# Optimization experiments

Hardware: AMD Instinct MI355X
Metric: run time of the kernel (lower is better)

The kernel has to match this reference:

```python
import jax, jax.numpy as jnp
import numpy as np

B, M, D = 8192, 64, 256
NEG = -1e9  # masking value for invalid (padded) memory slots


def setup_inputs() -> dict:
    key = jax.random.key(0)
    ks = jax.random.split(key, 8)
    s = 1.0 / np.sqrt(D)  # nn.Linear default init scale
    return {
        "h_tilde": jax.random.normal(ks[0], (B, D), jnp.float32),
        "mem": jax.random.normal(ks[1], (B, M, D), jnp.float32),
        "lengths": jax.random.randint(ks[2], (B,), 0, M + 1, jnp.int32),
        "Wg_w": jax.random.uniform(ks[3], (D, D), jnp.float32, -s, s),
        "Wg_b": jax.random.uniform(ks[4], (D,), jnp.float32, -s, s),
        "Ug_w": jax.random.uniform(ks[5], (D, D), jnp.float32, -s, s),
        "Ug_b": jax.random.uniform(ks[6], (D,), jnp.float32, -s, s),
        "b_g": jnp.zeros((D,), jnp.float32),
    }


def reference(h_tilde, mem, lengths, Wg_w, Wg_b, Ug_w, Ug_b, b_g):
    # valid-slot mask: [B, M]
    valid = jnp.arange(M)[None, :] < lengths[:, None]
    # per-sample attention over ragged memory
    scores = jnp.einsum("bmd,bd->bm", mem, h_tilde)          # [B, M]
    attn = jax.nn.softmax(jnp.where(valid, scores, NEG), axis=1)
    r = jnp.einsum("bm,bmd->bd", attn, mem)                   # [B, D]
    # gated fusion (two Linears + extra bias)
    g = jax.nn.sigmoid(h_tilde @ Wg_w.T + Wg_b + r @ Ug_w.T + Ug_b + b_g)
    fused = g * r + (1.0 - g) * h_tilde
    # empty-memory samples pass through h_tilde unchanged
    has_mem = (lengths > 0)[:, None]
    return jnp.where(has_mem, fused, h_tilde)
```

## Files before the change

### kernel.cpp

```cpp
#include <hip/hip_runtime.h>
#include <hip/hip_bf16.h>

#define BB 8192
#define MM 64
#define DD 256
#define NEGV -1e9f

__global__ __launch_bounds__(256) void attn_kernel(
    const float* __restrict__ h, const float* __restrict__ mem,
    const int* __restrict__ len, float* __restrict__ r_out)
{
    __shared__ __hip_bfloat16 tile[MM * DD];
    __shared__ float score_s[MM];
    __shared__ float attn_s[MM];

    const int b    = blockIdx.x;
    const int t    = threadIdx.x;
    const int lane = t & 63;
    const int wave = t >> 6;
    const int L    = len[b];

    const float4 hv = *reinterpret_cast<const float4*>(h + (size_t)b * DD + 4 * lane);
    const float* mbase = mem + (size_t)b * MM * DD;

    #pragma unroll
    for (int i = 0; i < 16; ++i) {
        const int m = wave * 16 + i;
        const float4 v = *reinterpret_cast<const float4*>(mbase + m * DD + 4 * lane);

        __hip_bfloat162* t2 =
            reinterpret_cast<__hip_bfloat162*>(tile + m * DD + 4 * lane);
        __hip_bfloat162 p0, p1;
        p0.x = __float2bfloat16(v.x); p0.y = __float2bfloat16(v.y);
        p1.x = __float2bfloat16(v.z); p1.y = __float2bfloat16(v.w);
        t2[0] = p0; t2[1] = p1;

        float p = v.x * hv.x + v.y * hv.y + v.z * hv.z + v.w * hv.w;
        #pragma unroll
        for (int off = 32; off > 0; off >>= 1)
            p += __shfl_xor(p, off, 64);
        if (lane == 0) score_s[m] = (m < L) ? p : NEGV;
    }
    __syncthreads();

    if (wave == 0) {
        const float s = score_s[lane];
        float mx = s;
        #pragma unroll
        for (int off = 32; off > 0; off >>= 1)
            mx = fmaxf(mx, __shfl_xor(mx, off, 64));
        const float e = __expf(s - mx);
        float den = e;
        #pragma unroll
        for (int off = 32; off > 0; off >>= 1)
            den += __shfl_xor(den, off, 64);
        attn_s[lane] = e / den;
    }
    __syncthreads();

    float acc = 0.f;
    #pragma unroll
    for (int m = 0; m < MM; ++m)
        acc += attn_s[m] * __bfloat162float(tile[m * DD + t]);
    r_out[(size_t)b * DD + t] = acc;
}

__global__ __launch_bounds__(256) void gate_kernel(
    const float* __restrict__ h, const float* __restrict__ r,
    const int* __restrict__ len,
    const float* __restrict__ Wg_w, const float* __restrict__ Wg_b,
    const float* __restrict__ Ug_w, const float* __restrict__ Ug_b,
    const float* __restrict__ b_g, float* __restrict__ out)
{
    __shared__ float As[64][33];
    __shared__ float Ws[64][33];

    const int t     = threadIdx.x;
    const int brow0 = blockIdx.x * 64;
    const int dcol0 = blockIdx.y * 64;
    const int ty = t >> 4;
    const int tx = t & 15;

    const int lrow = t >> 3;
    const int lc4  = (t & 7) * 4;

    float acc[4][4] = {};

    for (int phase = 0; phase < 2; ++phase) {
        const float* A = phase ? r : h;
        const float* W = phase ? Ug_w : Wg_w;
        for (int k0 = 0; k0 < DD; k0 += 32) {
            #pragma unroll
            for (int half = 0; half < 2; ++half) {
                const int row = lrow + 32 * half;
                const float4 av = *reinterpret_cast<const float4*>(
                    A + (size_t)(brow0 + row) * DD + k0 + lc4);
                As[row][lc4 + 0] = av.x; As[row][lc4 + 1] = av.y;
                As[row][lc4 + 2] = av.z; As[row][lc4 + 3] = av.w;
                const float4 wv = *reinterpret_cast<const float4*>(
                    W + (size_t)(dcol0 + row) * DD + k0 + lc4);
                Ws[row][lc4 + 0] = wv.x; Ws[row][lc4 + 1] = wv.y;
                Ws[row][lc4 + 2] = wv.z; Ws[row][lc4 + 3] = wv.w;
            }
            __syncthreads();
            #pragma unroll
            for (int kk = 0; kk < 32; ++kk) {
                float a[4], w[4];
                #pragma unroll
                for (int i = 0; i < 4; ++i) a[i] = As[4 * ty + i][kk];
                #pragma unroll
                for (int j = 0; j < 4; ++j) w[j] = Ws[4 * tx + j][kk];
                #pragma unroll
                for (int i = 0; i < 4; ++i)
                    #pragma unroll
                    for (int j = 0; j < 4; ++j)
                        acc[i][j] += a[i] * w[j];
            }
            __syncthreads();
        }
    }

    #pragma unroll
    for (int i = 0; i < 4; ++i) {
        const int bb = brow0 + 4 * ty + i;
        const int lb = len[bb];
        #pragma unroll
        for (int j = 0; j < 4; ++j) {
            const int d = dcol0 + 4 * tx + j;
            const float x = acc[i][j] + Wg_b[d] + Ug_b[d] + b_g[d];
            const float g = 1.f / (1.f + __expf(-x));
            const size_t idx = (size_t)bb * DD + d;
            const float rv = r[idx];
            const float hv = h[idx];
            out[idx] = (lb > 0) ? (g * rv + (1.f - g) * hv) : hv;
        }
    }
}

extern "C" void kernel_launch(void* const* d_in, const int* in_sizes, int n_in,
                              void* d_out, int out_size, void* d_ws, size_t ws_size,
                              hipStream_t stream) {
    const float* h    = (const float*)d_in[0];
    const float* mem  = (const float*)d_in[1];
    const int*   len  = (const int*)d_in[2];
    const float* Wg_w = (const float*)d_in[3];
    const float* Wg_b = (const float*)d_in[4];
    const float* Ug_w = (const float*)d_in[5];
    const float* Ug_b = (const float*)d_in[6];
    const float* b_g  = (const float*)d_in[7];
    float* out  = (float*)d_out;
    float* r_ws = (float*)d_ws;

    attn_kernel<<<BB, 256, 0, stream>>>(h, mem, len, r_ws);
    gate_kernel<<<dim3(BB / 64, DD / 64), 256, 0, stream>>>(
        h, r_ws, len, Wg_w, Wg_b, Ug_w, Ug_b, b_g, out);
}
```

Baseline: 757.5 us.

## Use bf16 MFMA for gate GEMM and restructure attention loads

```diff
diff --git a/kernel.cpp b/kernel.cpp
--- a/kernel.cpp
+++ b/kernel.cpp
@@ -5,46 +5,57 @@
 #define MM 64
 #define DD 256
 #define NEGV -1e9f
+#define TSTR 260
+
+typedef __attribute__((ext_vector_type(8))) short frag_ab;
+typedef __attribute__((ext_vector_type(4))) float f32x4;
+
+struct __align__(8) bfq { __hip_bfloat162 lo, hi; };
+
+__device__ inline short f2bs(float f) {
+    __hip_bfloat16 v = __float2bfloat16(f);
+    return *reinterpret_cast<short*>(&v);
+}
 
 __global__ __launch_bounds__(256) void attn_kernel(
     const float* __restrict__ h, const float* __restrict__ mem,
     const int* __restrict__ len, float* __restrict__ r_out)
 {
-    __shared__ __hip_bfloat16 tile[MM * DD];
+    __shared__ __hip_bfloat16 tile[MM * TSTR];
+    __shared__ __align__(16) float h_s[DD];
     __shared__ float score_s[MM];
-    __shared__ float attn_s[MM];
+    __shared__ __align__(16) float attn_s[MM];
 
-    const int b    = blockIdx.x;
-    const int t    = threadIdx.x;
-    const int lane = t & 63;
-    const int wave = t >> 6;
-    const int L    = len[b];
+    const int b = blockIdx.x;
+    const int t = threadIdx.x;
+    const int m = t >> 2;
+    const int c = t & 3;
+    const int L = len[b];
 
-    const float4 hv = *reinterpret_cast<const float4*>(h + (size_t)b * DD + 4 * lane);
-    const float* mbase = mem + (size_t)b * MM * DD;
-
-    #pragma unroll
-    for (int i = 0; i < 16; ++i) {
-        const int m = wave * 16 + i;
-        const float4 v = *reinterpret_cast<const float4*>(mbase + m * DD + 4 * lane);
-
-        __hip_bfloat162* t2 =
-            reinterpret_cast<__hip_bfloat162*>(tile + m * DD + 4 * lane);
-        __hip_bfloat162 p0, p1;
-        p0.x = __float2bfloat16(v.x); p0.y = __float2bfloat16(v.y);
-        p1.x = __float2bfloat16(v.z); p1.y = __float2bfloat16(v.w);
-        t2[0] = p0; t2[1] = p1;
-
-        float p = v.x * hv.x + v.y * hv.y + v.z * hv.z + v.w * hv.w;
-        #pragma unroll
-        for (int off = 32; off > 0; off >>= 1)
-            p += __shfl_xor(p, off, 64);
-        if (lane == 0) score_s[m] = (m < L) ? p : NEGV;
-    }
+    h_s[t] = h[(size_t)b * DD + t];
     __syncthreads();
 
-    if (wave == 0) {
-        const float s = score_s[lane];
+    const float* mrow = mem + (size_t)b * MM * DD + (size_t)m * DD + c * 64;
+    __hip_bfloat16* trow = tile + m * TSTR + c * 64;
+
+    float p = 0.f;
+    #pragma unroll
+    for (int j = 0; j < 16; ++j) {
+        const float4 v  = *reinterpret_cast<const float4*>(mrow + 4 * j);
+        const float4 hv = *reinterpret_cast<const float4*>(h_s + c * 64 + 4 * j);
+        p += v.x * hv.x + v.y * hv.y + v.z * hv.z + v.w * hv.w;
+        bfq q;
+        q.lo = __float22bfloat162_rn(float2{v.x, v.y});
+        q.hi = __float22bfloat162_rn(float2{v.z, v.w});
+        *reinterpret_cast<bfq*>(trow + 4 * j) = q;
+    }
+    p += __shfl_xor(p, 1, 64);
+    p += __shfl_xor(p, 2, 64);
+    if (c == 0) score_s[m] = (m < L) ? p : NEGV;
+    __syncthreads();
+
+    if (t < 64) {
+        const float s = score_s[t];
         float mx = s;
         #pragma unroll
         for (int off = 32; off > 0; off >>= 1)
@@ -54,14 +65,19 @@
         #pragma unroll
         for (int off = 32; off > 0; off >>= 1)
             den += __shfl_xor(den, off, 64);
-        attn_s[lane] = e / den;
+        attn_s[t] = e / den;
     }
     __syncthreads();
 
     float acc = 0.f;
     #pragma unroll
-    for (int m = 0; m < MM; ++m)
-        acc += attn_s[m] * __bfloat162float(tile[m * DD + t]);
+    for (int mc = 0; mc < 16; ++mc) {
+        const float4 aw = *reinterpret_cast<const float4*>(attn_s + 4 * mc);
+        acc += aw.x * __bfloat162float(tile[(4 * mc + 0) * TSTR + t]);
+        acc += aw.y * __bfloat162float(tile[(4 * mc + 1) * TSTR + t]);
+        acc += aw.z * __bfloat162float(tile[(4 * mc + 2) * TSTR + t]);
+        acc += aw.w * __bfloat162float(tile[(4 * mc + 3) * TSTR + t]);
+    }
     r_out[(size_t)b * DD + t] = acc;
 }
 
@@ -72,67 +88,79 @@
     const float* __restrict__ Ug_w, const float* __restrict__ Ug_b,
     const float* __restrict__ b_g, float* __restrict__ out)
 {
-    __shared__ float As[64][33];
-    __shared__ float Ws[64][33];
+    __shared__ __hip_bfloat16 Abuf[64 * 32];
+    __shared__ __hip_bfloat16 Wbuf[64 * 32];
 
-    const int t     = threadIdx.x;
+    const int t    = threadIdx.x;
+    const int lane = t & 63;
+    const int wave = t >> 6;
     const int brow0 = blockIdx.x * 64;
     const int dcol0 = blockIdx.y * 64;
-    const int ty = t >> 4;
-    const int tx = t & 15;
 
-    const int lrow = t >> 3;
-    const int lc4  = (t & 7) * 4;
+    const int srow = t >> 2;
+    const int skq  = t & 3;
 
-    float acc[4][4] = {};
+    const f32x4 zero = {0.f, 0.f, 0.f, 0.f};
+    f32x4 acc[4];
+    #pragma unroll
+    for (int ct = 0; ct < 4; ++ct) acc[ct] = zero;
+
+    const int arow_m = (lane & 15);
+    const int kchunk = (lane >> 4) * 8;
 
     for (int phase = 0; phase < 2; ++phase) {
-        const float* A = phase ? r : h;
-        const float* W = phase ? Ug_w : Wg_w;
+        const float* Ag = phase ? r : h;
+        const float* Wg = phase ? Ug_w : Wg_w;
+        const float* ap = Ag + (size_t)(brow0 + srow) * DD + skq * 8;
+        const float* wp = Wg + (size_t)(dcol0 + srow) * DD + skq * 8;
+
         for (int k0 = 0; k0 < DD; k0 += 32) {
+            const float4 a0 = *reinterpret_cast<const float4*>(ap + k0);
+            const float4 a1 = *reinterpret_cast<const float4*>(ap + k0 + 4);
+            const float4 w0 = *reinterpret_cast<const float4*>(wp + k0);
+            const float4 w1 = *reinterpret_cast<const float4*>(wp + k0 + 4);
+
+            __syncthreads();
+            frag_ab av, wv;
+            av[0] = f2bs(a0.x); av[1] = f2bs(a0.y); av[2] = f2bs(a0.z); av[3] = f2bs(a0.w);
+            av[4] = f2bs(a1.x); av[5] = f2bs(a1.y); av[6] = f2bs(a1.z); av[7] = f2bs(a1.w);
+            wv[0] = f2bs(w0.x); wv[1] = f2bs(w0.y); wv[2] = f2bs(w0.z); wv[3] = f2bs(w0.w);
+            wv[4] = f2bs(w1.x); wv[5] = f2bs(w1.y); wv[6] = f2bs(w1.z); wv[7] = f2bs(w1.w);
+            *reinterpret_cast<frag_ab*>(&Abuf[srow * 32 + skq * 8]) = av;
+            *reinterpret_cast<frag_ab*>(&Wbuf[srow * 32 + skq * 8]) = wv;
+            __syncthreads();
+
+            const frag_ab af = *reinterpret_cast<const frag_ab*>(
+                &Abuf[(wave * 16 + arow_m) * 32 + kchunk]);
             #pragma unroll
-            for (int half = 0; half < 2; ++half) {
-                const int row = lrow + 32 * half;
-                const float4 av = *reinterpret_cast<const float4*>(
-                    A + (size_t)(brow0 + row) * DD + k0 + lc4);
-                As[row][lc4 + 0] = av.x; As[row][lc4 + 1] = av.y;
-                As[row][lc4 + 2] = av.z; As[row][lc4 + 3] = av.w;
-                const float4 wv = *reinterpret_cast<const float4*>(
-                    W + (size_t)(dcol0 + row) * DD + k0 + lc4);
-                Ws[row][lc4 + 0] = wv.x; Ws[row][lc4 + 1] = wv.y;
-                Ws[row][lc4 + 2] = wv.z; Ws[row][lc4 + 3] = wv.w;
+            for (int ct = 0; ct < 4; ++ct) {
+                const frag_ab wf = *reinterpret_cast<const frag_ab*>(
+                    &Wbuf[(ct * 16 + arow_m) * 32 + kchunk]);
+                acc[ct] = __builtin_amdgcn_mfma_f32_16x16x32_bf16(af, wf, acc[ct], 0, 0, 0);
             }
-            __syncthreads();
-            #pragma unroll
-            for (int kk = 0; kk < 32; ++kk) {
-                float a[4], w[4];
-                #pragma unroll
-                for (int i = 0; i < 4; ++i) a[i] = As[4 * ty + i][kk];
-                #pragma unroll
-                for (int j = 0; j < 4; ++j) w[j] = Ws[4 * tx + j][kk];
-                #pragma unroll
-                for (int i = 0; i < 4; ++i)
-                    #pragma unroll
-                    for (int j = 0; j < 4; ++j)
-                        acc[i][j] += a[i] * w[j];
-            }
-            __syncthreads();
         }
     }
 
+    float bias_v[4];
+    #pragma unroll
+    for (int ct = 0; ct < 4; ++ct) {
+        const int d = dcol0 + ct * 16 + (lane & 15);
+        bias_v[ct] = Wg_b[d] + Ug_b[d] + b_g[d];
+    }
+    const int rbase = brow0 + wave * 16 + (lane >> 4) * 4;
     #pragma unroll
     for (int i = 0; i < 4; ++i) {
-        const int bb = brow0 + 4 * ty + i;
+        const int bb = rbase + i;
         const int lb = len[bb];
         #pragma unroll
-        for (int j = 0; j < 4; ++j) {
-            const int d = dcol0 + 4 * tx + j;
-            const float x = acc[i][j] + Wg_b[d] + Ug_b[d] + b_g[d];
+        for (int ct = 0; ct < 4; ++ct) {
+            const int d = dcol0 + ct * 16 + (lane & 15);
+            const float x = acc[ct][i] + bias_v[ct];
             const float g = 1.f / (1.f + __expf(-x));
             const size_t idx = (size_t)bb * DD + d;
             const float rv = r[idx];
             const float hv = h[idx];
-            out[idx] = (lb > 0) ? (g * rv + (1.f - g) * hv) : hv;
+            out[idx] = (lb > 0) ? (hv + g * (rv - hv)) : hv;
         }
     }
 }
```

After: 715.6 us. -5.5%, faster.
